# Kernel tuning notes

Measured on AMD Instinct MI355X. Metric: run time of the kernel, lower is better.

The kernel has to match this reference:

```python
import jax, jax.numpy as jnp
from jax import lax
import numpy as np

B, T, D_IN = 1024, 64, 1662
H1, H2, H3 = 64, 128, 64


def _lstm_layer(x, w_ih, w_hh, b_ih, b_hh):
    """PyTorch-convention single-layer LSTM. x: [B,T,D]; gate order i,f,g,o."""
    Bc = x.shape[0]
    H = w_hh.shape[1]
    # Precompute input contribution for all timesteps: [B,T,4H]
    xg = jnp.einsum('btd,gd->btg', x, w_ih) + b_ih + b_hh

    def step(carry, xt):
        h, c = carry
        gates = xt + h @ w_hh.T  # [B,4H]
        i, f, g, o = jnp.split(gates, 4, axis=-1)
        i = jax.nn.sigmoid(i)
        f = jax.nn.sigmoid(f)
        g = jnp.tanh(g)
        o = jax.nn.sigmoid(o)
        c = f * c + i * g
        h = o * jnp.tanh(c)
        return (h, c), h

    h0 = jnp.zeros((Bc, H), x.dtype)
    (_, _), hs = lax.scan(step, (h0, h0), jnp.swapaxes(xg, 0, 1))
    return jnp.swapaxes(hs, 0, 1)  # [B,T,H]


def setup_inputs() -> dict:
    key = jax.random.key(0)
    ks = jax.random.split(key, 20)

    def u(k, shape, fan):
        bound = 1.0 / np.sqrt(fan)
        return jax.random.uniform(k, shape, jnp.float32, -bound, bound)

    x = jax.random.normal(ks[0], (B, T, D_IN), jnp.float32)
    return {
        'x': x,
        'w_ih1': u(ks[1], (4 * H1, D_IN), H1), 'w_hh1': u(ks[2], (4 * H1, H1), H1),
        'b_ih1': u(ks[3], (4 * H1,), H1),      'b_hh1': u(ks[4], (4 * H1,), H1),
        'w_ih2': u(ks[5], (4 * H2, H1), H2),   'w_hh2': u(ks[6], (4 * H2, H2), H2),
        'b_ih2': u(ks[7], (4 * H2,), H2),      'b_hh2': u(ks[8], (4 * H2,), H2),
        'w_ih3': u(ks[9], (4 * H3, H2), H3),   'w_hh3': u(ks[10], (4 * H3, H3), H3),
        'b_ih3': u(ks[11], (4 * H3,), H3),     'b_hh3': u(ks[12], (4 * H3,), H3),
        'fc1_w': u(ks[13], (64, 64), 64),      'fc1_b': u(ks[14], (64,), 64),
        'fc2_w': u(ks[15], (32, 64), 64),      'fc2_b': u(ks[16], (32,), 64),
        'fc3_w': u(ks[17], (3, 32), 32),       'fc3_b': u(ks[18], (3,), 32),
    }


def reference(x, w_ih1, w_hh1, b_ih1, b_hh1,
              w_ih2, w_hh2, b_ih2, b_hh2,
              w_ih3, w_hh3, b_ih3, b_hh3,
              fc1_w, fc1_b, fc2_w, fc2_b, fc3_w, fc3_b):
    h = _lstm_layer(x, w_ih1, w_hh1, b_ih1, b_hh1)   # [B,T,64]
    h = _lstm_layer(h, w_ih2, w_hh2, b_ih2, b_hh2)   # [B,T,128]
    h = _lstm_layer(h, w_ih3, w_hh3, b_ih3, b_hh3)   # [B,T,64]
    h = h[:, -1, :]                                   # [B,64]
    h = jax.nn.relu(h @ fc1_w.T + fc1_b)
    h = jax.nn.relu(h @ fc2_w.T + fc2_b)
    return jax.nn.softmax(h @ fc3_w.T + fc3_b, axis=1)  # [B,3]
```

## Files before the change

kernel.cpp:

```cpp
#include <hip/hip_runtime.h>
#include <hip/hip_bf16.h>

#define B_SZ   1024
#define T_SZ   64
#define D_IN   1662
#define D_INP  1664
#define M_SZ   (B_SZ * T_SZ)

typedef __attribute__((ext_vector_type(8))) short short8;
typedef __attribute__((ext_vector_type(4))) float f32x4;
typedef unsigned short ushort_t;

__device__ __forceinline__ unsigned short f2bf(float f) {
    unsigned u = __builtin_bit_cast(unsigned, f);
    u += 0x7FFFu + ((u >> 16) & 1u);
    return (unsigned short)(u >> 16);
}
__device__ __forceinline__ float bf2f(ushort_t u) {
    return __builtin_bit_cast(float, (unsigned)u << 16);
}

#define GLD16(gp, lp) __builtin_amdgcn_global_load_lds(                        \
    (const __attribute__((address_space(1))) void*)(gp),                       \
    (__attribute__((address_space(3))) void*)(lp), 16, 0, 0)

__device__ __forceinline__ float sigmoid_f(float x) {
    return 1.0f / (1.0f + __expf(-x));
}
__device__ __forceinline__ float tanh_f(float x) {
    float a = fabsf(x);
    float e = __expf(2.0f * a);
    float r = 1.0f - 2.0f / (e + 1.0f);
    return copysignf(r, x);
}

__global__ __launch_bounds__(256) void convert_w1(
    const float* __restrict__ src, ushort_t* __restrict__ dst)
{
    constexpr int cpr = D_INP >> 3;
    const int total = 256 * cpr;
    const int stride = gridDim.x * blockDim.x;
    for (int idx = blockIdx.x * blockDim.x + threadIdx.x;
         idx < total; idx += stride) {
        const int row  = idx / cpr;
        const int base = (idx % cpr) << 3;
        const float* s = src + (size_t)row * D_IN;
        short8 o;
        #pragma unroll
        for (int j = 0; j < 4; ++j) {
            const int k = base + 2 * j;
            float2 v = make_float2(0.f, 0.f);
            if (k < D_IN) v = *(const float2*)(s + k);
            o[2 * j]     = (short)f2bf(v.x);
            o[2 * j + 1] = (short)f2bf(v.y);
        }
        *(short8*)(dst + (size_t)row * D_INP + base) = o;
    }
}

__global__ __launch_bounds__(256, 4) void gemm_l1(
    const float* __restrict__ A, const ushort_t* __restrict__ W,
    ushort_t* __restrict__ out)
{
    constexpr int K = D_IN, Kp = D_INP, G = 256;
    __shared__ __align__(16) ushort_t As[64 * 32];
    __shared__ __align__(16) ushort_t Ws[256 * 32];

    const int tid = threadIdx.x, lane = tid & 63, wid = tid >> 6;
    const int m0 = blockIdx.x * 64;

    const int arow  = tid >> 2;
    const int acolb = (tid & 3) * 8;
    const float* Abase = A + (size_t)(m0 + arow) * K + acolb;

    const size_t wlofs = (size_t)(lane >> 2) * Kp + (lane & 3) * 8;
    const ushort_t* Wg0 = W + (size_t)(wid * 64) * Kp + wlofs;
    const ushort_t* Wg1 = Wg0 + (size_t)16 * Kp;
    const ushort_t* Wg2 = Wg0 + (size_t)32 * Kp;
    const ushort_t* Wg3 = Wg0 + (size_t)48 * Kp;
    ushort_t* lw0 = &Ws[(wid * 64) * 32];
    ushort_t* lw1 = lw0 + 16 * 32;
    ushort_t* lw2 = lw0 + 32 * 32;
    ushort_t* lw3 = lw0 + 48 * 32;

    const int fr = lane & 15, kq = (lane >> 4) * 8;

    f32x4 acc[4][4] = {};
    const int nFull = K / 32;

    float2 av[4];
    #pragma unroll
    for (int j = 0; j < 4; ++j) av[j] = *(const float2*)(Abase + 2 * j);

    for (int it = 0; it <= nFull; ++it) {
        const int k0 = it * 32;
        __syncthreads();
        GLD16(Wg0 + k0, lw0); GLD16(Wg1 + k0, lw1);
        GLD16(Wg2 + k0, lw2); GLD16(Wg3 + k0, lw3);
        short8 pk;
        #pragma unroll
        for (int j = 0; j < 4; ++j) {
            pk[2 * j]     = (short)f2bf(av[j].x);
            pk[2 * j + 1] = (short)f2bf(av[j].y);
        }
        *(short8*)&As[arow * 32 + acolb] = pk;
        __syncthreads();

        if (it < nFull) {
            const int kn = (it + 1) * 32;
            if (it + 1 < nFull) {
                #pragma unroll
                for (int j = 0; j < 4; ++j)
                    av[j] = *(const float2*)(Abase + kn + 2 * j);
            } else {
                #pragma unroll
                for (int j = 0; j < 4; ++j) {
                    const int kk = kn + acolb + 2 * j;
                    av[j] = (kk < K) ? *(const float2*)(Abase + kn + 2 * j)
                                     : make_float2(0.f, 0.f);
                }
            }
        }

        short8 af[4], bfr[4];
        #pragma unroll
        for (int fm = 0; fm < 4; ++fm)
            af[fm] = *(const short8*)&As[(fm * 16 + fr) * 32 + kq];
        #pragma unroll
        for (int fn = 0; fn < 4; ++fn)
            bfr[fn] = *(const short8*)&Ws[(wid * 64 + fn * 16 + fr) * 32 + kq];
        #pragma unroll
        for (int fm = 0; fm < 4; ++fm)
            #pragma unroll
            for (int fn = 0; fn < 4; ++fn)
                acc[fm][fn] = __builtin_amdgcn_mfma_f32_16x16x32_bf16(
                    af[fm], bfr[fn], acc[fm][fn], 0, 0, 0);
    }

    const int rbase = (lane >> 4) * 4;
    #pragma unroll
    for (int fn = 0; fn < 4; ++fn) {
        const int g = wid * 64 + fn * 16 + fr;
        #pragma unroll
        for (int fm = 0; fm < 4; ++fm) {
            const int mbase = m0 + fm * 16 + rbase;
            #pragma unroll
            for (int j = 0; j < 4; ++j)
                out[(size_t)(mbase + j) * G + g] = f2bf(acc[fm][fn][j]);
        }
    }
}

__global__ __launch_bounds__(512, 2) void lstm3_pipe(
    const ushort_t* __restrict__ xg1,
    const float* __restrict__ whh1,
    const float* __restrict__ bih1, const float* __restrict__ bhh1,
    const float* __restrict__ wih2, const float* __restrict__ whh2,
    const float* __restrict__ bih2, const float* __restrict__ bhh2,
    const float* __restrict__ wih3, const float* __restrict__ whh3,
    const float* __restrict__ bih3, const float* __restrict__ bhh3,
    float* __restrict__ hlast, int Tn)
{
    __shared__ ushort_t h1sh[2][16 * 64];
    __shared__ ushort_t h2sh[2][16 * 128];
    __shared__ ushort_t h3sh[2][16 * 64];
    __shared__ ushort_t xsh[2][4 * 256];
    __shared__ float    gsh[4][1024];
    __shared__ float    bsh[1024];

    const int tid = threadIdx.x, lane = tid & 63, wid = tid >> 6;
    const int r0 = blockIdx.x * 4;
    const int fr = lane & 15, hi = lane >> 4, kq = hi * 8;

    int role, uw;
    if (wid < 2)      { role = 1; uw = wid * 32; }
    else if (wid < 6) { role = 2; uw = (wid - 2) * 32; }
    else              { role = 3; uw = (wid - 6) * 32; }

    short8 bregB[2][4][2];
    short8 bregA[2][4][4];
    #pragma unroll
    for (int ut = 0; ut < 2; ++ut)
        #pragma unroll
        for (int g = 0; g < 4; ++g) {
            const int uu = uw + ut * 16 + fr;
            const float *pB, *pA = nullptr;
            if (role == 1)      { pB = whh1 + (size_t)(g * 64 + uu) * 64; }
            else if (role == 2) { pB = wih2 + (size_t)(g * 128 + uu) * 64;
                                  pA = whh2 + (size_t)(g * 128 + uu) * 128; }
            else                { pB = whh3 + (size_t)(g * 64 + uu) * 64;
                                  pA = wih3 + (size_t)(g * 64 + uu) * 128; }
            #pragma unroll
            for (int ks = 0; ks < 2; ++ks) {
                short8 b;
                #pragma unroll
                for (int j = 0; j < 8; ++j)
                    b[j] = (short)f2bf(pB[ks * 32 + kq + j]);
                bregB[ut][g][ks] = b;
            }
            if (role >= 2) {
                #pragma unroll
                for (int ks = 0; ks < 4; ++ks) {
                    short8 b;
                    #pragma unroll
                    for (int j = 0; j < 8; ++j)
                        b[j] = (short)f2bf(pA[ks * 32 + kq + j]);
                    bregA[ut][g][ks] = b;
                }
            }
        }

    for (int i = tid; i < 1024; i += 512) {
        float bv;
        if (i < 256)      bv = bih1[i] + bhh1[i];
        else if (i < 768) bv = bih2[i - 256] + bhh2[i - 256];
        else              bv = bih3[i - 768] + bhh3[i - 768];
        bsh[i] = bv;
        h1sh[0][i] = 0; h1sh[1][i] = 0;
        h3sh[0][i] = 0; h3sh[1][i] = 0;
    }
    for (int i = tid; i < 2048; i += 512) { h2sh[0][i] = 0; h2sh[1][i] = 0; }

    if (tid < 128) {
        const int rw = tid >> 5, xc = (tid & 31) * 8;
        *(short8*)&xsh[0][rw * 256 + xc] =
            *(const short8*)(xg1 + ((size_t)(r0 + rw) * Tn) * 256 + xc);
    }

    float c[2] = {0.f, 0.f};
    __syncthreads();

    const int nSteps = Tn + 2;
    for (int s = 0; s < nSteps; ++s) {
        const int rb = s & 1, wb = rb ^ 1;

        short8 xr;
        const bool doX = (tid < 128) && (s + 1 < Tn);
        if (doX) {
            const int rw = tid >> 5, xc = (tid & 31) * 8;
            xr = *(const short8*)(xg1 +
                 ((size_t)(r0 + rw) * Tn + (s + 1)) * 256 + xc);
        }

        const bool act = (role == 1) ? (s < Tn)
                       : (role == 2) ? (s >= 1 && s <= Tn)
                                     : (s >= 2 && s <= Tn + 1);
        if (act) {
            short8 a2r[2], a4r[4];
            const ushort_t* src2 = (role == 3) ? h3sh[rb] : h1sh[rb];
            #pragma unroll
            for (int ks = 0; ks < 2; ++ks) {
                const int k0 = ks * 32 + kq;
                a2r[ks] = *(const short8*)&src2[fr * 64 + (k0 ^ ((fr & 7) << 3))];
            }
            if (role >= 2) {
                #pragma unroll
                for (int ks = 0; ks < 4; ++ks) {
                    const int k0 = ks * 32 + kq;
                    a4r[ks] = *(const short8*)
                        &h2sh[rb][fr * 128 + (k0 ^ ((fr & 7) << 3))];
                }
            }
            const int sec = (role == 1) ? 0 : (role == 2) ? 256 : 768;
            const int Hl  = (role == 2) ? 128 : 64;
            #pragma unroll
            for (int ut = 0; ut < 2; ++ut)
                #pragma unroll
                for (int g = 0; g < 4; ++g) {
                    f32x4 acc = {};
                    #pragma unroll
                    for (int ks = 0; ks < 2; ++ks)
                        acc = __builtin_amdgcn_mfma_f32_16x16x32_bf16(
                            a2r[ks], bregB[ut][g][ks], acc, 0, 0, 0);
                    if (role >= 2) {
                        #pragma unroll
                        for (int ks = 0; ks < 4; ++ks)
                            acc = __builtin_amdgcn_mfma_f32_16x16x32_bf16(
                                a4r[ks], bregA[ut][g][ks], acc, 0, 0, 0);
                    }
                    if (hi == 0) {
                        const int col = sec + g * Hl + uw + ut * 16 + fr;
                        #pragma unroll
                        for (int j = 0; j < 4; ++j)
                            gsh[j][col] = acc[j];
                    }
                }
        }
        __syncthreads();

        #pragma unroll
        for (int i = 0; i < 2; ++i) {
            const int item = tid + i * 512;
            const int row = item >> 8, ug = item & 255;
            int u, Hl, sec, tt, lay;
            if (ug < 64)       { lay = 1; u = ug;       Hl = 64;  sec = 0;   tt = s; }
            else if (ug < 192) { lay = 2; u = ug - 64;  Hl = 128; sec = 256; tt = s - 1; }
            else               { lay = 3; u = ug - 192; Hl = 64;  sec = 768; tt = s - 2; }
            if (tt >= 0 && tt < Tn) {
                const int col0 = sec + u;
                float gi = gsh[row][col0]          + bsh[col0];
                float gf = gsh[row][col0 + Hl]     + bsh[col0 + Hl];
                float gg = gsh[row][col0 + 2 * Hl] + bsh[col0 + 2 * Hl];
                float go = gsh[row][col0 + 3 * Hl] + bsh[col0 + 3 * Hl];
                if (lay == 1) {
                    const ushort_t* xb = &xsh[s & 1][row * 256 + u];
                    gi += bf2f(xb[0]);   gf += bf2f(xb[64]);
                    gg += bf2f(xb[128]); go += bf2f(xb[192]);
                }
                const float iv = sigmoid_f(gi);
                const float fv = sigmoid_f(gf);
                const float gv = tanh_f(gg);
                const float ov = sigmoid_f(go);
                c[i] = fmaf(fv, c[i], iv * gv);
                const float h = ov * tanh_f(c[i]);
                ushort_t* hdst = (lay == 1) ? h1sh[wb]
                               : (lay == 2) ? h2sh[wb] : h3sh[wb];
                hdst[row * Hl + (u ^ (row << 3))] = f2bf(h);
                if (lay == 3 && tt == Tn - 1)
                    hlast[(size_t)(r0 + row) * 64 + u] = h;
            }
        }

        if (doX) {
            const int rw = tid >> 5, xc = (tid & 31) * 8;
            *(short8*)&xsh[(s + 1) & 1][rw * 256 + xc] = xr;
        }
        __syncthreads();
    }
}

__global__ __launch_bounds__(256) void head_kernel(
    const float* __restrict__ hlast,
    const float* __restrict__ w1, const float* __restrict__ b1,
    const float* __restrict__ w2, const float* __restrict__ b2,
    const float* __restrict__ w3, const float* __restrict__ b3,
    float* __restrict__ out)
{
    __shared__ float W1[64][64];
    __shared__ float W2[32][64];
    __shared__ float W3[3][32];
    __shared__ float hin[16][64];
    __shared__ float a1[16][64];
    __shared__ float a2[16][32];
    __shared__ float lg[16][3];

    const int tid = threadIdx.x;
    const int r0 = blockIdx.x * 16;

    for (int i = tid; i < 64 * 64; i += 256) W1[i >> 6][i & 63] = w1[i];
    for (int i = tid; i < 32 * 64; i += 256) W2[i >> 6][i & 63] = w2[i];
    for (int i = tid; i < 3 * 32; i += 256) W3[i >> 5][i & 31] = w3[i];
    for (int i = tid; i < 16 * 64; i += 256) {
        int r = i >> 6, u = i & 63;
        hin[r][u] = hlast[(size_t)(r0 + r) * 64 + u];
    }
    __syncthreads();

    for (int i = tid; i < 16 * 64; i += 256) {
        int r = i >> 6, j = i & 63;
        float s = b1[j];
        #pragma unroll
        for (int k = 0; k < 64; ++k) s = fmaf(hin[r][k], W1[j][k], s);
        a1[r][j] = fmaxf(s, 0.f);
    }
    __syncthreads();

    for (int i = tid; i < 16 * 32; i += 256) {
        int r = i >> 5, j = i & 31;
        float s = b2[j];
        #pragma unroll
        for (int k = 0; k < 64; ++k) s = fmaf(a1[r][k], W2[j][k], s);
        a2[r][j] = fmaxf(s, 0.f);
    }
    __syncthreads();

    for (int i = tid; i < 16 * 3; i += 256) {
        int r = i / 3, j = i % 3;
        float s = b3[j];
        #pragma unroll
        for (int k = 0; k < 32; ++k) s = fmaf(a2[r][k], W3[j][k], s);
        lg[r][j] = s;
    }
    __syncthreads();

    if (tid < 16) {
        float l0 = lg[tid][0], l1 = lg[tid][1], l2 = lg[tid][2];
        float m = fmaxf(l0, fmaxf(l1, l2));
        float e0 = __expf(l0 - m), e1 = __expf(l1 - m), e2 = __expf(l2 - m);
        float inv = 1.0f / (e0 + e1 + e2);
        out[(size_t)(r0 + tid) * 3 + 0] = e0 * inv;
        out[(size_t)(r0 + tid) * 3 + 1] = e1 * inv;
        out[(size_t)(r0 + tid) * 3 + 2] = e2 * inv;
    }
}

extern "C" void kernel_launch(void* const* d_in, const int* in_sizes, int n_in,
                              void* d_out, int out_size, void* d_ws, size_t ws_size,
                              hipStream_t stream)
{
    const float* x    = (const float*)d_in[0];
    const float* wih1 = (const float*)d_in[1];
    const float* whh1 = (const float*)d_in[2];
    const float* bih1 = (const float*)d_in[3];
    const float* bhh1 = (const float*)d_in[4];
    const float* wih2 = (const float*)d_in[5];
    const float* whh2 = (const float*)d_in[6];
    const float* bih2 = (const float*)d_in[7];
    const float* bhh2 = (const float*)d_in[8];
    const float* wih3 = (const float*)d_in[9];
    const float* whh3 = (const float*)d_in[10];
    const float* bih3 = (const float*)d_in[11];
    const float* bhh3 = (const float*)d_in[12];
    const float* f1w  = (const float*)d_in[13];
    const float* f1b  = (const float*)d_in[14];
    const float* f2w  = (const float*)d_in[15];
    const float* f2b  = (const float*)d_in[16];
    const float* f3w  = (const float*)d_in[17];
    const float* f3b  = (const float*)d_in[18];
    float* outp = (float*)d_out;

    char* wsb = (char*)d_ws;
    size_t off = 0;
    ushort_t* bufA  = (ushort_t*)(wsb + off); off += 33554432;
    float*    hlast = (float*)(wsb + off);    off += 262144;
    ushort_t* w1b   = (ushort_t*)(wsb + off);

    const int T = T_SZ;

    convert_w1<<<208, 256, 0, stream>>>(wih1, w1b);

    gemm_l1<<<M_SZ / 64, 256, 0, stream>>>(x, w1b, bufA);

    lstm3_pipe<<<B_SZ / 4, 512, 0, stream>>>(
        bufA, whh1, bih1, bhh1,
        wih2, whh2, bih2, bhh2,
        wih3, whh3, bih3, bhh3,
        hlast, T);

    head_kernel<<<B_SZ / 16, 256, 0, stream>>>(
        hlast, f1w, f1b, f2w, f2b, f3w, f3b, outp);
}
```

Baseline: 371.7 us.

## Double-buffer LDS tiles and prefetch two steps ahead in layer-1 GEMM

The layer-1 input GEMM now keeps two LDS buffers for the A and W tiles. The W tile for the next step is issued via global_load_lds, and A registers are prefetched two k-steps ahead, with explicit vmcnt waits and a single barrier per iteration in place of two. The A tail read is clamped with min() rather than a branch, though the clamp yields a duplicated value rather than zero for the padded columns. Launch bounds drop to 3 blocks/CU for the GEMM and 1 for the LSTM kernel, giving more registers at the cost of occupancy.

```diff
diff --git a/kernel.cpp b/kernel.cpp
--- a/kernel.cpp
+++ b/kernel.cpp
@@ -58,13 +58,14 @@
     }
 }
 
-__global__ __launch_bounds__(256, 4) void gemm_l1(
+__global__ __launch_bounds__(256, 3) void gemm_l1(
     const float* __restrict__ A, const ushort_t* __restrict__ W,
     ushort_t* __restrict__ out)
 {
     constexpr int K = D_IN, Kp = D_INP, G = 256;
-    __shared__ __align__(16) ushort_t As[64 * 32];
-    __shared__ __align__(16) ushort_t Ws[256 * 32];
+    constexpr int NIT = 52;
+    __shared__ __align__(16) ushort_t As[2][64 * 32];
+    __shared__ __align__(16) ushort_t Ws[2][256 * 32];
 
     const int tid = threadIdx.x, lane = tid & 63, wid = tid >> 6;
     const int m0 = blockIdx.x * 64;
@@ -72,70 +73,85 @@
     const int arow  = tid >> 2;
     const int acolb = (tid & 3) * 8;
     const float* Abase = A + (size_t)(m0 + arow) * K + acolb;
+    const int kmax = K - 2 - acolb;
 
     const size_t wlofs = (size_t)(lane >> 2) * Kp + (lane & 3) * 8;
-    const ushort_t* Wg0 = W + (size_t)(wid * 64) * Kp + wlofs;
-    const ushort_t* Wg1 = Wg0 + (size_t)16 * Kp;
-    const ushort_t* Wg2 = Wg0 + (size_t)32 * Kp;
-    const ushort_t* Wg3 = Wg0 + (size_t)48 * Kp;
-    ushort_t* lw0 = &Ws[(wid * 64) * 32];
-    ushort_t* lw1 = lw0 + 16 * 32;
-    ushort_t* lw2 = lw0 + 32 * 32;
-    ushort_t* lw3 = lw0 + 48 * 32;
+    const ushort_t* WgBase = W + (size_t)(wid * 64) * Kp + wlofs;
 
     const int fr = lane & 15, kq = (lane >> 4) * 8;
 
     f32x4 acc[4][4] = {};
-    const int nFull = K / 32;
-
-    float2 av[4];
+    float2 av0[4], av1[4];
+
     #pragma unroll
-    for (int j = 0; j < 4; ++j) av[j] = *(const float2*)(Abase + 2 * j);
-
-    for (int it = 0; it <= nFull; ++it) {
-        const int k0 = it * 32;
-        __syncthreads();
-        GLD16(Wg0 + k0, lw0); GLD16(Wg1 + k0, lw1);
-        GLD16(Wg2 + k0, lw2); GLD16(Wg3 + k0, lw3);
-        short8 pk;
-        #pragma unroll
-        for (int j = 0; j < 4; ++j) {
-            pk[2 * j]     = (short)f2bf(av[j].x);
-            pk[2 * j + 1] = (short)f2bf(av[j].y);
-        }
-        *(short8*)&As[arow * 32 + acolb] = pk;
-        __syncthreads();
-
-        if (it < nFull) {
-            const int kn = (it + 1) * 32;
-            if (it + 1 < nFull) {
-                #pragma unroll
-                for (int j = 0; j < 4; ++j)
-                    av[j] = *(const float2*)(Abase + kn + 2 * j);
-            } else {
-                #pragma unroll
-                for (int j = 0; j < 4; ++j) {
-                    const int kk = kn + acolb + 2 * j;
-                    av[j] = (kk < K) ? *(const float2*)(Abase + kn + 2 * j)
-                                     : make_float2(0.f, 0.f);
-                }
-            }
-        }
-
-        short8 af[4], bfr[4];
-        #pragma unroll
-        for (int fm = 0; fm < 4; ++fm)
-            af[fm] = *(const short8*)&As[(fm * 16 + fr) * 32 + kq];
-        #pragma unroll
-        for (int fn = 0; fn < 4; ++fn)
-            bfr[fn] = *(const short8*)&Ws[(wid * 64 + fn * 16 + fr) * 32 + kq];
-        #pragma unroll
-        for (int fm = 0; fm < 4; ++fm)
-            #pragma unroll
-            for (int fn = 0; fn < 4; ++fn)
-                acc[fm][fn] = __builtin_amdgcn_mfma_f32_16x16x32_bf16(
-                    af[fm], bfr[fn], acc[fm][fn], 0, 0, 0);
-    }
+    for (int j = 0; j < 4; ++j)
+        av0[j] = *(const float2*)(Abase + 2 * j);
+    __builtin_amdgcn_sched_barrier(0);
+    #pragma unroll
+    for (int c = 0; c < 4; ++c)
+        GLD16(WgBase + (size_t)(c * 16) * Kp,
+              &Ws[0][(wid * 64 + c * 16) * 32]);
+    __builtin_amdgcn_sched_barrier(0);
+    #pragma unroll
+    for (int j = 0; j < 4; ++j)
+        av1[j] = *(const float2*)(Abase + min(32 + 2 * j, kmax));
+    __builtin_amdgcn_sched_barrier(0);
+    asm volatile("s_waitcnt vmcnt(4)" ::: "memory");
+
+#define L1_ITER(T, AV)                                                         \
+  do {                                                                         \
+    const int bcur = (T) & 1;                                                  \
+    short8 pk;                                                                 \
+    _Pragma("unroll")                                                          \
+    for (int j = 0; j < 4; ++j) {                                              \
+        pk[2 * j]     = (short)f2bf(AV[j].x);                                  \
+        pk[2 * j + 1] = (short)f2bf(AV[j].y);                                  \
+    }                                                                          \
+    *(short8*)&As[bcur][arow * 32 + acolb] = pk;                               \
+    asm volatile("s_waitcnt lgkmcnt(0)" ::: "memory");                         \
+    __builtin_amdgcn_s_barrier();                                              \
+    __builtin_amdgcn_sched_barrier(0);                                         \
+    if ((T) + 1 < NIT) {                                                       \
+        const size_t kw = (size_t)((T) + 1) * 32;                              \
+        _Pragma("unroll")                                                      \
+        for (int c = 0; c < 4; ++c)                                            \
+            GLD16(WgBase + (size_t)(c * 16) * Kp + kw,                         \
+                  &Ws[((T) + 1) & 1][(wid * 64 + c * 16) * 32]);               \
+    }                                                                          \
+    __builtin_amdgcn_sched_barrier(0);                                         \
+    if ((T) + 2 < NIT) {                                                       \
+        const int kA = ((T) + 2) * 32;                                         \
+        _Pragma("unroll")                                                      \
+        for (int j = 0; j < 4; ++j)                                            \
+            AV[j] = *(const float2*)(Abase + min(kA + 2 * j, kmax));           \
+    }                                                                          \
+    __builtin_amdgcn_sched_barrier(0);                                         \
+    {                                                                          \
+        short8 af[4], bfr[4];                                                  \
+        _Pragma("unroll")                                                      \
+        for (int fm = 0; fm < 4; ++fm)                                         \
+            af[fm] = *(const short8*)&As[bcur][(fm * 16 + fr) * 32 + kq];      \
+        _Pragma("unroll")                                                      \
+        for (int fn = 0; fn < 4; ++fn)                                         \
+            bfr[fn] = *(const short8*)                                         \
+                &Ws[bcur][(wid * 64 + fn * 16 + fr) * 32 + kq];                \
+        _Pragma("unroll")                                                      \
+        for (int fm = 0; fm < 4; ++fm)                                         \
+            _Pragma("unroll")                                                  \
+            for (int fn = 0; fn < 4; ++fn)                                     \
+                acc[fm][fn] = __builtin_amdgcn_mfma_f32_16x16x32_bf16(         \
+                    af[fm], bfr[fn], acc[fm][fn], 0, 0, 0);                    \
+    }                                                                          \
+    __builtin_amdgcn_sched_barrier(0);                                         \
+    if ((T) < NIT - 2) asm volatile("s_waitcnt vmcnt(4)" ::: "memory");        \
+    else               asm volatile("s_waitcnt vmcnt(0)" ::: "memory");        \
+  } while (0)
+
+    for (int tt = 0; tt < NIT / 2; ++tt) {
+        L1_ITER(2 * tt,     av0);
+        L1_ITER(2 * tt + 1, av1);
+    }
+#undef L1_ITER
 
     const int rbase = (lane >> 4) * 4;
     #pragma unroll
@@ -151,7 +167,7 @@
     }
 }
 
-__global__ __launch_bounds__(512, 2) void lstm3_pipe(
+__global__ __launch_bounds__(512, 1) void lstm3_pipe(
     const ushort_t* __restrict__ xg1,
     const float* __restrict__ whh1,
     const float* __restrict__ bih1, const float* __restrict__ bhh1,
```

Measured after the change: 393.6 us. 1.06x slower.
